# Optimization experiments

Hardware: AMD Instinct MI355X
Metric: run time of the kernel (lower is better)

## Reference

```python
import jax, jax.numpy as jnp
import numpy as np

D_MODEL = 1024; D_STATE = 64; D_CONV = 4; EXPAND = 2; HEADDIM = 128; NGROUPS = 1; CHUNK = 256
D_INNER = EXPAND * D_MODEL            # 2048
NHEADS = D_INNER // HEADDIM           # 16
CONV_DIM = D_INNER + 2 * NGROUPS * D_STATE   # 2176
D_IN_PROJ = 2 * D_INNER + 2 * NGROUPS * D_STATE + NHEADS  # 4240
B = 4; G = 256; L = 2048
EPS = 1e-5


def setup_inputs() -> dict:
    key = jax.random.key(0)
    ks = jax.random.split(key, 12)
    def nrm(k, shape, s=0.02):
        return jax.random.normal(k, shape, jnp.float32) * s
    return dict(
        local_repr=jax.random.normal(ks[0], (B, L, D_MODEL), jnp.float32),
        global_repr=jax.random.normal(ks[1], (B, G, D_MODEL), jnp.float32),
        norm1_w=jnp.ones((D_MODEL,), jnp.float32), norm1_b=jnp.zeros((D_MODEL,), jnp.float32),
        norm2_w=jnp.ones((D_MODEL,), jnp.float32), norm2_b=jnp.zeros((D_MODEL,), jnp.float32),
        norm3_w=jnp.ones((D_MODEL,), jnp.float32), norm3_b=jnp.zeros((D_MODEL,), jnp.float32),
        in_proj_w=nrm(ks[2], (D_IN_PROJ, D_MODEL)),
        conv_w=nrm(ks[3], (CONV_DIM, D_CONV), 0.2),
        conv_b=jnp.zeros((CONV_DIM,), jnp.float32),
        dt_bias=jnp.log(jnp.expm1(jax.random.uniform(ks[4], (NHEADS,), jnp.float32, 1e-3, 0.1))),
        A_log=jnp.log(jax.random.uniform(ks[5], (NHEADS,), jnp.float32, 1.0, 16.0)),
        D_skip=jnp.ones((NHEADS,), jnp.float32),
        ssd_norm_w=jnp.ones((D_INNER,), jnp.float32),
        out_proj_w=nrm(ks[6], (D_MODEL, D_INNER)),
        ffn_w1=nrm(ks[7], (D_MODEL // 2, D_MODEL)),
        ffn_b1=jnp.zeros((D_MODEL // 2,), jnp.float32),
        ffn_w2=nrm(ks[8], (D_MODEL, D_MODEL // 2)),
        ffn_b2=jnp.zeros((D_MODEL,), jnp.float32),
    )


def _ln(x, w, b):
    mu = jnp.mean(x, axis=-1, keepdims=True)
    var = jnp.mean((x - mu) ** 2, axis=-1, keepdims=True)
    return (x - mu) * jax.lax.rsqrt(var + EPS) * w + b


def _segsum(a):
    # a: (..., T) -> (..., T, T) lower-triangular sums a[j+1..i]
    T = a.shape[-1]
    cs = jnp.cumsum(a, axis=-1)
    diff = cs[..., :, None] - cs[..., None, :]
    mask = jnp.tril(jnp.ones((T, T), bool))
    return jnp.where(mask, diff, -jnp.inf)


def _ssd(xdt, a_dt, Bh, Ch):
    # xdt: (b,t,h,p) = x*dt ; a_dt: (b,t,h) = dt*A ; Bh,Ch: (b,t,h,n)
    b, t, h, p = xdt.shape
    n = Bh.shape[-1]
    c = t // CHUNK
    X = xdt.reshape(b, c, CHUNK, h, p)
    Bc = Bh.reshape(b, c, CHUNK, h, n)
    Cc = Ch.reshape(b, c, CHUNK, h, n)
    Ac = a_dt.reshape(b, c, CHUNK, h).transpose(0, 3, 1, 2)  # (b,h,c,k)
    A_cum = jnp.cumsum(Ac, axis=-1)
    Lm = jnp.exp(_segsum(Ac))                                # (b,h,c,k,k)
    Y_diag = jnp.einsum('bckhn,bcshn,bhcks,bcshp->bckhp', Cc, Bc, Lm, X)
    decay_states = jnp.exp(A_cum[..., -1:] - A_cum)          # (b,h,c,k)
    states = jnp.einsum('bckhn,bhck,bckhp->bchpn', Bc, decay_states, X)
    A_last = jnp.pad(A_cum[..., -1], ((0, 0), (0, 0), (1, 0)))
    decay_chunk = jnp.exp(_segsum(A_last))                   # (b,h,c+1,c+1)
    states = jnp.concatenate([jnp.zeros_like(states[:, :1]), states], axis=1)
    new_states = jnp.einsum('bhzc,bchpn->bzhpn', decay_chunk, states)
    states_in = new_states[:, :-1]                           # (b,c,h,p,n)
    out_decay = jnp.exp(A_cum)                               # (b,h,c,k)
    Y_off = jnp.einsum('bckhn,bchpn,bhck->bckhp', Cc, states_in, out_decay)
    return (Y_diag + Y_off).reshape(b, t, h, p)


def _mamba2(x, in_proj_w, conv_w, conv_b, dt_bias, A_log, D_skip, ssd_norm_w, out_proj_w):
    b, t, _ = x.shape
    zxbcdt = x @ in_proj_w.T                                  # (b,t,D_IN_PROJ)
    z = zxbcdt[..., :D_INNER]
    xBC = zxbcdt[..., D_INNER:D_INNER + CONV_DIM]
    dt = jax.nn.softplus(zxbcdt[..., D_INNER + CONV_DIM:] + dt_bias)  # (b,t,h)
    # causal depthwise conv1d, kernel D_CONV
    xp = jnp.pad(xBC, ((0, 0), (D_CONV - 1, 0), (0, 0)))
    xBC = sum(xp[:, i:i + t, :] * conv_w[:, i] for i in range(D_CONV)) + conv_b
    xBC = jax.nn.silu(xBC)
    xs = xBC[..., :D_INNER].reshape(b, t, NHEADS, HEADDIM)
    Bm = xBC[..., D_INNER:D_INNER + NGROUPS * D_STATE].reshape(b, t, NGROUPS, D_STATE)
    Cm = xBC[..., D_INNER + NGROUPS * D_STATE:].reshape(b, t, NGROUPS, D_STATE)
    rep = NHEADS // NGROUPS
    Bh = jnp.repeat(Bm, rep, axis=2)
    Ch = jnp.repeat(Cm, rep, axis=2)
    A = -jnp.exp(A_log)                                       # (h,)
    Y = _ssd(xs * dt[..., None], dt * A, Bh, Ch)
    y = Y + D_skip[None, None, :, None] * xs
    y = y.reshape(b, t, D_INNER)
    # gated RMSNorm (norm_before_gate=False)
    y = y * jax.nn.silu(z)
    y = y * jax.lax.rsqrt(jnp.mean(y * y, axis=-1, keepdims=True) + EPS) * ssd_norm_w
    return y @ out_proj_w.T


def reference(local_repr, global_repr, norm1_w, norm1_b, norm2_w, norm2_b, norm3_w, norm3_b,
              in_proj_w, conv_w, conv_b, dt_bias, A_log, D_skip, ssd_norm_w, out_proj_w,
              ffn_w1, ffn_b1, ffn_w2, ffn_b2):
    local_n = _ln(local_repr, norm1_w, norm1_b)
    global_n = _ln(global_repr, norm2_w, norm2_b)
    x = jnp.concatenate([global_n, local_n], axis=1)          # (B, G+L, D)
    x = _mamba2(x, in_proj_w, conv_w, conv_b, dt_bias, A_log, D_skip, ssd_norm_w, out_proj_w)
    x = x[:, -local_n.shape[1]:, :] + local_n
    x = _ln(x, norm3_w, norm3_b)
    h = jax.nn.gelu(x @ ffn_w1.T + ffn_b1, approximate=False)
    return (h @ ffn_w2.T + ffn_b2) + x
```

## Files before the change

### kernel.cpp

```cpp
#include <hip/hip_runtime.h>
#include <math.h>

#define B_ 4
#define L_ 2048
#define G_ 256
#define T_ 2304
#define DM 1024
#define DINNER 2048
#define NH 16
#define HD 128
#define NSTATE 64
#define CONVD 2176
#define DPROJ 4240
#define NPROJ_PAD 4352
#define NCHUNK 9
#define CK 256
#define EPSV 1e-5f
#define CROWS 16
#define CONVBLKS 612

typedef unsigned short bf16t;
using bf16x8 = __attribute__((ext_vector_type(8))) short;
using f32x4  = __attribute__((ext_vector_type(4))) float;

__device__ __forceinline__ float bf2f(bf16t u) {
  return __uint_as_float(((unsigned int)u) << 16);
}
__device__ __forceinline__ bf16t f2bf(float f) {
  unsigned int u = __float_as_uint(f);
  u += 0x7FFFu + ((u >> 16) & 1u);
  return (bf16t)(u >> 16);
}

__device__ __forceinline__ void g2lds16(const bf16t* g, short* l) {
  __builtin_amdgcn_global_load_lds(
      (const __attribute__((address_space(1))) unsigned int*)g,
      (__attribute__((address_space(3))) unsigned int*)l, 16, 0, 0);
}

__device__ __forceinline__ int2 xcd_swz(int tiles_n) {
  int gx = gridDim.x, gy = gridDim.y;
  int id = blockIdx.y * gx + blockIdx.x;
  int cpx = (gx * gy) >> 3;
  int L = (id & 7) * cpx + (id >> 3);
  return make_int2(L % tiles_n, L / tiles_n);
}

__device__ __forceinline__ float2 block_reduce2(float a, float b) {
  __shared__ float sa[4], sb[4];
  #pragma unroll
  for (int off = 32; off > 0; off >>= 1) {
    a += __shfl_down(a, off, 64);
    b += __shfl_down(b, off, 64);
  }
  int lane = threadIdx.x & 63, wid = threadIdx.x >> 6;
  if (lane == 0) { sa[wid] = a; sb[wid] = b; }
  __syncthreads();
  return make_float2(sa[0] + sa[1] + sa[2] + sa[3], sb[0] + sb[1] + sb[2] + sb[3]);
}

__global__ __launch_bounds__(256) void ln_cvt_kernel(
    const float* __restrict__ localr, const float* __restrict__ globalr,
    const float* __restrict__ w1, const float* __restrict__ b1,
    const float* __restrict__ w2, const float* __restrict__ b2,
    bf16t* __restrict__ x, const float* __restrict__ inpw,
    bf16t* __restrict__ inpw_bf) {
  int blk = blockIdx.x;
  if (blk < B_ * T_) {
    int t = blk % T_, b = blk / T_;
    const float *src, *w, *bb;
    if (t < G_) { src = globalr + ((long)b * G_ + t) * DM;        w = w2; bb = b2; }
    else        { src = localr  + ((long)b * L_ + (t - G_)) * DM; w = w1; bb = b1; }
    int d = threadIdx.x * 4;
    float4 v = *(const float4*)&src[d];
    float s = v.x + v.y + v.z + v.w;
    float sq = v.x * v.x + v.y * v.y + v.z * v.z + v.w * v.w;
    float2 r2 = block_reduce2(s, sq);
    float mu = r2.x * (1.f / DM);
    float var = r2.y * (1.f / DM) - mu * mu;
    float rstd = rsqrtf(var + EPSV);
    float4 wv = *(const float4*)&w[d];
    float4 bv = *(const float4*)&bb[d];
    ushort4 o;
    o.x = f2bf((v.x - mu) * rstd * wv.x + bv.x);
    o.y = f2bf((v.y - mu) * rstd * wv.y + bv.y);
    o.z = f2bf((v.z - mu) * rstd * wv.z + bv.z);
    o.w = f2bf((v.w - mu) * rstd * wv.w + bv.w);
    *(ushort4*)&x[(long)blk * DM + d] = o;
  } else {
    long i = (long)(blk - B_ * T_) * 1024 + threadIdx.x * 4;
    const long nreal = (long)DPROJ * DM, ntot = (long)NPROJ_PAD * DM;
    if (i < ntot) {
      ushort4 o = {0, 0, 0, 0};
      if (i < nreal) {
        float4 v = *(const float4*)&inpw[i];
        o.x = f2bf(v.x); o.y = f2bf(v.y); o.z = f2bf(v.z); o.w = f2bf(v.w);
      }
      *(ushort4*)&inpw_bf[i] = o;
    }
  }
}

template<int EPI, bool OFFS, int K>
__global__ __launch_bounds__(512, 4) void gemm_wide(
    const bf16t* __restrict__ A, const bf16t* __restrict__ W,
    bf16t* __restrict__ Cb, bf16t* __restrict__ z, bf16t* __restrict__ xpre,
    float* __restrict__ dtr, const float* __restrict__ bias,
    const bf16t* __restrict__ res, float* __restrict__ Cf, int N) {
  __shared__ short LDS8[36864];
  int tid = threadIdx.x;
  int lane = tid & 63, w = tid >> 6;
  int wm = w >> 1, wn = w & 1;
  int l15 = lane & 15;
  int2 sz = xcd_swz(gridDim.x);
  int bn = sz.x * 128, bm = sz.y * 256;
  if (EPI == 0 && bn < DINNER && (bm % 2304) == 0) return;
  long bmA = OFFS ? ((long)(bm >> 11) * T_ + G_ + (bm & 2047)) : (long)bm;

  int csub = ((lane & 3) ^ ((lane >> 3) & 3)) * 8;
  const bf16t* srcA = A + (bmA + w * 16 + (lane >> 2)) * (long)K + csub;
  const bf16t* srcW = W + (long)(bn + w * 16 + (lane >> 2)) * K + csub;
  int stageDst = w * 512 + lane * 8;

  int off0 = l15 * 32 + (((lane >> 4) ^ ((l15 >> 1) & 3))) * 8;

  f32x4 acc[4][4] = {};
  bf16x8 af[4], bq[4];

#define STAGEA(gsrc, ldsoff) do { \
    g2lds16((gsrc), LDS8 + (ldsoff) + stageDst); \
    g2lds16((gsrc) + 128 * (long)K, LDS8 + (ldsoff) + stageDst + 4096); } while (0)
#define STAGEB(gsrc, ldsoff) g2lds16((gsrc), LDS8 + (ldsoff) + stageDst)

  STAGEA(srcA, 0);
  STAGEB(srcW, 24576);
  STAGEA(srcA + 32, 8192);
  STAGEB(srcW + 32, 24576 + 4096);
  asm volatile("s_waitcnt vmcnt(3)" ::: "memory");
  __builtin_amdgcn_s_barrier();

  const int nt = K >> 5;
  for (int t = 0; t < nt; ++t) {
    const short* aB = LDS8 + (t % 3) * 8192 + wm * 2048;
    const short* bB = LDS8 + 24576 + (t % 3) * 4096 + wn * 2048;
    int nsA = ((t + 2) % 3) * 8192;
    int nsB = 24576 + ((t + 2) % 3) * 4096;

    if (t + 2 < nt) {
      STAGEA(srcA + (t + 2) * 32, nsA);
      STAGEB(srcW + (t + 2) * 32, nsB);
    }
    #pragma unroll
    for (int mi = 0; mi < 4; mi++) af[mi] = *(const bf16x8*)&aB[mi * 512 + off0];
    #pragma unroll
    for (int ni = 0; ni < 4; ni++) bq[ni] = *(const bf16x8*)&bB[ni * 512 + off0];
    __builtin_amdgcn_s_setprio(1);
    #pragma unroll
    for (int mi = 0; mi < 4; mi++)
      #pragma unroll
      for (int ni = 0; ni < 4; ni++)
        acc[mi][ni] = __builtin_amdgcn_mfma_f32_16x16x32_bf16(af[mi], bq[ni], acc[mi][ni], 0, 0, 0);
    __builtin_amdgcn_s_setprio(0);
    if (t + 2 < nt)      asm volatile("s_waitcnt vmcnt(3)" ::: "memory");
    else if (t + 1 < nt) asm volatile("s_waitcnt vmcnt(0)" ::: "memory");
    __builtin_amdgcn_s_barrier();
  }
#undef STAGEA
#undef STAGEB

  if (EPI == 0 && bn == 4224) {
    if (wn == 0) {
      #pragma unroll
      for (int mi = 0; mi < 4; mi++)
        #pragma unroll
        for (int r = 0; r < 4; r++) {
          int row = bm + wm * 64 + mi * 16 + (lane >> 4) * 4 + r;
          dtr[(long)row * NH + l15] = acc[mi][0][r];
        }
    }
    return;
  }

  if (EPI == 2) {
    float* Cs32 = (float*)LDS8;
    #pragma unroll
    for (int pass = 0; pass < 4; pass++) {
      __syncthreads();
      if (wm == pass) {
        #pragma unroll
        for (int mi = 0; mi < 4; mi++)
          #pragma unroll
          for (int ni = 0; ni < 4; ni++)
            #pragma unroll
            for (int r = 0; r < 4; r++)
              Cs32[(mi * 16 + (lane >> 4) * 4 + r) * 136 + wn * 64 + ni * 16 + l15] =
                  acc[mi][ni][r];
      }
      __syncthreads();
      #pragma unroll
      for (int q = 0; q < 2; q++) {
        int idx = q * 512 + tid;
        int row = idx >> 4, cg = (idx & 15) * 8;
        long grow = bm + pass * 64 + row; int gcol = bn + cg;
        float4 v0 = *(float4*)&Cs32[row * 136 + cg];
        float4 v1 = *(float4*)&Cs32[row * 136 + cg + 4];
        float4 b0 = *(const float4*)&bias[gcol];
        float4 b1 = *(const float4*)&bias[gcol + 4];
        bf16x8 rv = *(const bf16x8*)&res[grow * (long)N + gcol];
        v0.x += b0.x + bf2f((bf16t)rv[0]); v0.y += b0.y + bf2f((bf16t)rv[1]);
        v0.z += b0.z + bf2f((bf16t)rv[2]); v0.w += b0.w + bf2f((bf16t)rv[3]);
        v1.x += b1.x + bf2f((bf16t)rv[4]); v1.y += b1.y + bf2f((bf16t)rv[5]);
        v1.z += b1.z + bf2f((bf16t)rv[6]); v1.w += b1.w + bf2f((bf16t)rv[7]);
        *(float4*)&Cf[grow * (long)N + gcol] = v0;
        *(float4*)&Cf[grow * (long)N + gcol + 4] = v1;
      }
    }
    return;
  }

  bf16t* Cs = (bf16t*)LDS8;
  #pragma unroll
  for (int pass = 0; pass < 2; pass++) {
    __syncthreads();
    if ((wm >> 1) == pass) {
      #pragma unroll
      for (int mi = 0; mi < 4; mi++)
        #pragma unroll
        for (int ni = 0; ni < 4; ni++)
          #pragma unroll
          for (int r = 0; r < 4; r++)
            Cs[((wm & 1) * 64 + mi * 16 + (lane >> 4) * 4 + r) * 136 + wn * 64 + ni * 16 + l15] =
                f2bf(acc[mi][ni][r]);
    }
    __syncthreads();
    #pragma unroll
    for (int q = 0; q < 4; q++) {
      int idx = q * 512 + tid;
      int row = idx >> 4, cg = idx & 15;
      int gcol = bn + cg * 8;
      long grow = bm + pass * 128 + row;
      bf16x8 v = *(bf16x8*)&Cs[row * 136 + cg * 8];
      if (EPI == 0) {
        if (gcol < DINNER) *(bf16x8*)&z[grow * DINNER + gcol] = v;
        else               *(bf16x8*)&xpre[grow * CONVD + (gcol - DINNER)] = v;
      } else {
        *(bf16x8*)&Cb[grow * (long)N + gcol] = v;
      }
    }
  }
}

template<int EPI>
__global__ __launch_bounds__(256) void gemm_mfma(
    const bf16t* __restrict__ A, const bf16t* __restrict__ W,
    const float* __restrict__ bias, const bf16t* __restrict__ res,
    float* __restrict__ Cf, bf16t* __restrict__ Cb,
    int N, int K) {
  __shared__ __align__(16) short LDS[128 * 136];
  short* As = LDS;
  short* Ws = LDS + 128 * 32;
  int tid = threadIdx.x;
  int lane = tid & 63, w = tid >> 6;
  int wr = w >> 1, wc = w & 1;
  int2 sz = xcd_swz(gridDim.x);
  int bn = sz.x * 128, bm = sz.y * 128;

  int r1 = tid >> 2,         s1 = (((tid & 3) ^ ((r1 >> 1) & 3))) * 8;
  int r2 = (tid + 256) >> 2, s2 = (((tid & 3) ^ ((r2 >> 1) & 3))) * 8;
  const bf16t* gA1 = A + (long)(bm + r1) * K + s1;
  const bf16t* gA2 = A + (long)(bm + r2) * K + s2;
  const bf16t* gW1 = W + (long)(bn + r1) * K + s1;
  const bf16t* gW2 = W + (long)(bn + r2) * K + s2;
  short* lA1 = As + tid * 8;
  short* lA2 = As + (tid + 256) * 8;
  short* lW1 = Ws + tid * 8;
  short* lW2 = Ws + (tid + 256) * 8;

  int arow = wr * 64 + (lane & 15);
  int brow = wc * 64 + (lane & 15);
  int koff = (((lane >> 4) ^ (((lane & 15) >> 1) & 3))) * 8;

  f32x4 acc[4][4] = {};
  for (int k0 = 0; k0 < K; k0 += 32) {
    g2lds16(gA1 + k0, lA1);
    g2lds16(gA2 + k0, lA2);
    g2lds16(gW1 + k0, lW1);
    g2lds16(gW2 + k0, lW2);
    __syncthreads();
    bf16x8 af[4], bf[4];
    #pragma unroll
    for (int mi = 0; mi < 4; mi++) af[mi] = *(bf16x8*)&As[(arow + mi * 16) * 32 + koff];
    #pragma unroll
    for (int ni = 0; ni < 4; ni++) bf[ni] = *(bf16x8*)&Ws[(brow + ni * 16) * 32 + koff];
    #pragma unroll
    for (int mi = 0; mi < 4; mi++)
      #pragma unroll
      for (int ni = 0; ni < 4; ni++)
        acc[mi][ni] = __builtin_amdgcn_mfma_f32_16x16x32_bf16(af[mi], bf[ni], acc[mi][ni], 0, 0, 0);
    __syncthreads();
  }

  int rb = wr * 64 + (lane >> 4) * 4;
  int cb = wc * 64 + (lane & 15);

  __syncthreads();
  bf16t* Cs = (bf16t*)LDS;
  #pragma unroll
  for (int mi = 0; mi < 4; mi++)
    #pragma unroll
    for (int ni = 0; ni < 4; ni++)
      #pragma unroll
      for (int r = 0; r < 4; r++) {
        float v = acc[mi][ni][r];
        if (EPI == 2) {
          v += bias[bn + cb + ni * 16];
          v = 0.5f * v * (1.f + erff(v * 0.70710678118f));
        }
        Cs[(rb + mi * 16 + r) * 136 + cb + ni * 16] = f2bf(v);
      }
  __syncthreads();
  #pragma unroll
  for (int pass = 0; pass < 8; pass++) {
    int row = pass * 16 + (tid >> 4);
    int col = (tid & 15) * 8;
    bf16x8 vv = *(bf16x8*)&Cs[row * 136 + col];
    long grow = bm + row; int gcol = bn + col;
    *(bf16x8*)&Cb[grow * N + gcol] = vv;
  }
}

__global__ __launch_bounds__(256) void conv_cumsum_kernel(
    const bf16t* __restrict__ xpre, const float* __restrict__ cw,
    const float* __restrict__ cb, bf16t* __restrict__ out,
    const float* __restrict__ dtraw, const float* __restrict__ dt_bias,
    const float* __restrict__ A_log, float* __restrict__ dt,
    float* __restrict__ Acum) {
  if (blockIdx.x < CONVBLKS) {
    int gt = blockIdx.x * 256 + threadIdx.x;
    int cg = gt % 272; int rt = gt / 272;
    int c0 = cg * 8;
    long r0 = (long)rt * CROWS;
    int t0 = (int)(r0 % T_);

    float wreg[4][8];
    #pragma unroll
    for (int j = 0; j < 8; j++) {
      float4 wa = *(const float4*)&cw[(c0 + j) * 4];
      wreg[0][j] = wa.x; wreg[1][j] = wa.y; wreg[2][j] = wa.z; wreg[3][j] = wa.w;
    }
    float4 cb0 = *(const float4*)&cb[c0];
    float4 cb1 = *(const float4*)&cb[c0 + 4];
    float bias[8] = {cb0.x, cb0.y, cb0.z, cb0.w, cb1.x, cb1.y, cb1.z, cb1.w};

    bf16x8 win[4];
    #pragma unroll
    for (int i = 0; i < 3; i++) {
      if (t0 - 3 + i >= 0) win[i] = *(const bf16x8*)&xpre[(r0 - 3 + i) * CONVD + c0];
      else                 win[i] = bf16x8{0,0,0,0,0,0,0,0};
    }

    #pragma unroll
    for (int k = 0; k < CROWS; k++) {
      win[3] = *(const bf16x8*)&xpre[(r0 + k) * CONVD + c0];
      float acc[8];
      #pragma unroll
      for (int j = 0; j < 8; j++) acc[j] = bias[j];
      #pragma unroll
      for (int i = 0; i < 4; i++)
        #pragma unroll
        for (int j = 0; j < 8; j++)
          acc[j] += bf2f((bf16t)win[i][j]) * wreg[i][j];
      bf16x8 o;
      #pragma unroll
      for (int j = 0; j < 8; j++) {
        float s = acc[j] / (1.f + __expf(-acc[j]));
        o[j] = (short)f2bf(s);
      }
      *(bf16x8*)&out[(r0 + k) * CONVD + c0] = o;
      win[0] = win[1]; win[1] = win[2]; win[2] = win[3];
    }
  } else {
    int bid = blockIdx.x - CONVBLKS;
    int c = bid % NCHUNK; int hh = bid / NCHUNK;
    int h = hh % NH; int b = hh / NH;
    int k = threadIdx.x;
    float a = -__expf(A_log[h]);
    long t = (long)b * T_ + c * CK + k;
    float v0 = dtraw[t * NH + h] + dt_bias[h];
    float dtv = (v0 > 20.f) ? v0 : log1pf(__expf(v0));
    dt[t * NH + h] = dtv;
    float v = dtv * a;
    __shared__ float buf[2][CK];
    int cur = 0;
    buf[0][k] = v; __syncthreads();
    for (int off = 1; off < CK; off <<= 1) {
      float tv = buf[cur][k];
      if (k >= off) tv += buf[cur][k - off];
      buf[1 - cur][k] = tv; cur ^= 1; __syncthreads();
    }
    Acum[(long)bid * CK + k] = buf[cur][k];
  }
}

__global__ __launch_bounds__(256) void chunk_states_kernel(
    const bf16t* __restrict__ xbc, const float* __restrict__ dt,
    const float* __restrict__ Acum, float* __restrict__ cs) {
  int bid = blockIdx.x;
  int h = bid & 15; int bc = bid >> 4;
  int c = bc & 7; int b = bc >> 3;
  int tid = threadIdx.x;
  int lane = tid & 63, w = tid >> 6;
  long tch = (long)b * T_ + c * CK;
  int acb = ((b * NH + h) * NCHUNK + c) * CK;
  float Alast = Acum[acb + CK - 1];

  __shared__ bf16t Xt[128][72];
  __shared__ bf16t Bt[64][72];
  __shared__ float wkv[256];
  wkv[tid] = __expf(Alast - Acum[acb + tid]) * dt[(tch + tid) * NH + h];

  f32x4 acc[8] = {};
  for (int kb = 0; kb < 4; kb++) {
    int s0 = kb * 64;
    __syncthreads();
    for (int e = tid; e < 16 * 32; e += 256) {
      int s4 = (e & 15) * 4, p4 = e >> 4;
      const bf16t* base = &xbc[(tch + s0 + s4) * CONVD + h * HD + p4 * 4];
      ushort4 u0 = *(const ushort4*)(base);
      ushort4 u1 = *(const ushort4*)(base + CONVD);
      ushort4 u2 = *(const ushort4*)(base + 2 * CONVD);
      ushort4 u3 = *(const ushort4*)(base + 3 * CONVD);
      float w0 = wkv[s0 + s4], w1 = wkv[s0 + s4 + 1];
      float w2 = wkv[s0 + s4 + 2], w3 = wkv[s0 + s4 + 3];
      ushort4 pk;
      pk.x = f2bf(bf2f(u0.x) * w0); pk.y = f2bf(bf2f(u1.x) * w1);
      pk.z = f2bf(bf2f(u2.x) * w2); pk.w = f2bf(bf2f(u3.x) * w3);
      *(ushort4*)&Xt[p4 * 4 + 0][s4] = pk;
      pk.x = f2bf(bf2f(u0.y) * w0); pk.y = f2bf(bf2f(u1.y) * w1);
      pk.z = f2bf(bf2f(u2.y) * w2); pk.w = f2bf(bf2f(u3.y) * w3);
      *(ushort4*)&Xt[p4 * 4 + 1][s4] = pk;
      pk.x = f2bf(bf2f(u0.z) * w0); pk.y = f2bf(bf2f(u1.z) * w1);
      pk.z = f2bf(bf2f(u2.z) * w2); pk.w = f2bf(bf2f(u3.z) * w3);
      *(ushort4*)&Xt[p4 * 4 + 2][s4] = pk;
      pk.x = f2bf(bf2f(u0.w) * w0); pk.y = f2bf(bf2f(u1.w) * w1);
      pk.z = f2bf(bf2f(u2.w) * w2); pk.w = f2bf(bf2f(u3.w) * w3);
      *(ushort4*)&Xt[p4 * 4 + 3][s4] = pk;
    }
    for (int e = tid; e < 16 * 16; e += 256) {
      int s4 = (e & 15) * 4, n4 = e >> 4;
      const bf16t* base = &xbc[(tch + s0 + s4) * CONVD + DINNER + n4 * 4];
      ushort4 u0 = *(const ushort4*)(base);
      ushort4 u1 = *(const ushort4*)(base + CONVD);
      ushort4 u2 = *(const ushort4*)(base + 2 * CONVD);
      ushort4 u3 = *(const ushort4*)(base + 3 * CONVD);
      ushort4 pk;
      pk.x = u0.x; pk.y = u1.x; pk.z = u2.x; pk.w = u3.x;
      *(ushort4*)&Bt[n4 * 4 + 0][s4] = pk;
      pk.x = u0.y; pk.y = u1.y; pk.z = u2.y; pk.w = u3.y;
      *(ushort4*)&Bt[n4 * 4 + 1][s4] = pk;
      pk.x = u0.z; pk.y = u1.z; pk.z = u2.z; pk.w = u3.z;
      *(ushort4*)&Bt[n4 * 4 + 2][s4] = pk;
      pk.x = u0.w; pk.y = u1.w; pk.z = u2.w; pk.w = u3.w;
      *(ushort4*)&Bt[n4 * 4 + 3][s4] = pk;
    }
    __syncthreads();
    #pragma unroll
    for (int ks = 0; ks < 2; ks++) {
      int koff = (lane >> 4) * 8 + ks * 32;
      bf16x8 bfr = *(bf16x8*)&Bt[w * 16 + (lane & 15)][koff];
      #pragma unroll
      for (int mi = 0; mi < 8; mi++) {
        bf16x8 af = *(bf16x8*)&Xt[mi * 16 + (lane & 15)][koff];
        acc[mi] = __builtin_amdgcn_mfma_f32_16x16x32_bf16(af, bfr, acc[mi], 0, 0, 0);
      }
    }
  }
  int cbid = (b * NCHUNK + c) * NH + h;
  float* out = cs + (long)cbid * HD * NSTATE;
  int n = w * 16 + (lane & 15);
  #pragma unroll
  for (int mi = 0; mi < 8; mi++) {
    #pragma unroll
    for (int r = 0; r < 4; r++) {
      int p = mi * 16 + (lane >> 4) * 4 + r;
      out[p * NSTATE + n] = acc[mi][r];
    }
  }
}

__global__ __launch_bounds__(256) void state_pass_kernel(
    float* __restrict__ cs, const float* __restrict__ Acum) {
  int bh = blockIdx.x;
  int b = bh / NH, h = bh % NH;
  int e0 = blockIdx.y * 1024 + threadIdx.x;
  for (int q = 0; q < 4; q++) {
    int e = e0 + q * 256;
    float s = 0.f;
    for (int c = 0; c < NCHUNK; c++) {
      long idx = ((long)(b * NCHUNK + c) * NH + h) * (HD * NSTATE) + e;
      if (c < NCHUNK - 1) {
        float tmp = cs[idx];
        cs[idx] = s;
        float g = __expf(Acum[((b * NH + h) * NCHUNK + c) * CK + CK - 1]);
        s = s * g + tmp;
      } else {
        cs[idx] = s;
      }
    }
  }
}

__global__ __launch_bounds__(256) void ssd_y_kernel(
    const bf16t* __restrict__ xbc, const float* __restrict__ dt,
    const float* __restrict__ Acum, const float* __restrict__ sin_,
    const float* __restrict__ Dskip, bf16t* __restrict__ Y) {
  int bid = blockIdx.x;
  int h = bid & 15; int bc = bid >> 4;
  int c = 1 + (bc & 7); int b = bc >> 3;
  int rt = blockIdx.y;
  int tid = threadIdx.x;
  int lane = tid & 63, w = tid >> 6;
  int wr = w >> 1, wc = w & 1;
  long tch = (long)b * T_ + c * CK;
  long tbase = tch + rt * 128;
  int acb = ((b * NH + h) * NCHUNK + c) * CK;

  __shared__ bf16t Cs[128][72];
  __shared__ bf16t Bs[64][72];
  __shared__ __align__(16) bf16t XtSm[2][128][72];
  bf16t (*Xt)[72] = XtSm[0];
  bf16t (*Sm)[72] = XtSm[1];
  __shared__ float Acv[256];
  __shared__ float dtv[256];

  for (int e = tid; e < 128 * 8; e += 256) {
    int row = e >> 3, seg = (e & 7) * 8;
    *(bf16x8*)&Cs[row][seg] =
        *(const bf16x8*)&xbc[(tbase + row) * CONVD + DINNER + NSTATE + seg];
  }
  Acv[tid] = Acum[acb + tid];
  dtv[tid] = dt[(tch + tid) * NH + h];
  const float* Ak = Acv + rt * 128;

  f32x4 acc[4][4] = {};
  int nsb = 2 * (rt + 1);
  for (int sb = 0; sb < nsb; sb++) {
    int s0 = sb * 64;
    __syncthreads();
    for (int e = tid; e < 64 * 8; e += 256) {
      int row = e >> 3, seg = (e & 7) * 8;
      *(bf16x8*)&Bs[row][seg] =
          *(const bf16x8*)&xbc[(tch + s0 + row) * CONVD + DINNER + seg];
    }
    for (int e = tid; e < 16 * 32; e += 256) {
      int s4 = (e & 15) * 4, p4 = e >> 4;
      const bf16t* base = &xbc[(tch + s0 + s4) * CONVD + h * HD + p4 * 4];
      ushort4 u0 = *(const ushort4*)(base);
      ushort4 u1 = *(const ushort4*)(base + CONVD);
      ushort4 u2 = *(const ushort4*)(base + 2 * CONVD);
      ushort4 u3 = *(const ushort4*)(base + 3 * CONVD);
      float d0 = dtv[s0 + s4], d1 = dtv[s0 + s4 + 1];
      float d2 = dtv[s0 + s4 + 2], d3 = dtv[s0 + s4 + 3];
      ushort4 pk;
      pk.x = f2bf(bf2f(u0.x) * d0); pk.y = f2bf(bf2f(u1.x) * d1);
      pk.z = f2bf(bf2f(u2.x) * d2); pk.w = f2bf(bf2f(u3.x) * d3);
      *(ushort4*)&Xt[p4 * 4 + 0][s4] = pk;
      pk.x = f2bf(bf2f(u0.y) * d0); pk.y = f2bf(bf2f(u1.y) * d1);
      pk.z = f2bf(bf2f(u2.y) * d2); pk.w = f2bf(bf2f(u3.y) * d3);
      *(ushort4*)&Xt[p4 * 4 + 1][s4] = pk;
      pk.x = f2bf(bf2f(u0.z) * d0); pk.y = f2bf(bf2f(u1.z) * d1);
      pk.z = f2bf(bf2f(u2.z) * d2); pk.w = f2bf(bf2f(u3.z) * d3);
      *(ushort4*)&Xt[p4 * 4 + 2][s4] = pk;
      pk.x = f2bf(bf2f(u0.w) * d0); pk.y = f2bf(bf2f(u1.w) * d1);
      pk.z = f2bf(bf2f(u2.w) * d2); pk.w = f2bf(bf2f(u3.w) * d3);
      *(ushort4*)&Xt[p4 * 4 + 3][s4] = pk;
    }
    __syncthreads();
    {
      f32x4 sacc[2][4] = {};
      int rw0 = w * 32;
      #pragma unroll
      for (int ks = 0; ks < 2; ks++) {
        int koff = (lane >> 4) * 8 + ks * 32;
        bf16x8 a0 = *(bf16x8*)&Cs[rw0 + (lane & 15)][koff];
        bf16x8 a1 = *(bf16x8*)&Cs[rw0 + 16 + (lane & 15)][koff];
        #pragma unroll
        for (int ni = 0; ni < 4; ni++) {
          bf16x8 bfr = *(bf16x8*)&Bs[ni * 16 + (lane & 15)][koff];
          sacc[0][ni] = __builtin_amdgcn_mfma_f32_16x16x32_bf16(a0, bfr, sacc[0][ni], 0, 0, 0);
          sacc[1][ni] = __builtin_amdgcn_mfma_f32_16x16x32_bf16(a1, bfr, sacc[1][ni], 0, 0, 0);
        }
      }
      #pragma unroll
      for (int mi = 0; mi < 2; mi++) {
        #pragma unroll
        for (int ni = 0; ni < 4; ni++) {
          #pragma unroll
          for (int r = 0; r < 4; r++) {
            int row = rw0 + mi * 16 + (lane >> 4) * 4 + r;
            int scol = ni * 16 + (lane & 15);
            int kglob = rt * 128 + row;
            int sglob = s0 + scol;
            float val = 0.f;
            if (sglob <= kglob) val = sacc[mi][ni][r] * __expf(Ak[row] - Acv[s0 + scol]);
            Sm[row][scol] = f2bf(val);
          }
        }
      }
    }
    __syncthreads();
    #pragma unroll
    for (int ks = 0; ks < 2; ks++) {
      int koff = (lane >> 4) * 8 + ks * 32;
      bf16x8 af[4], bfr[4];
      #pragma unroll
      for (int mi = 0; mi < 4; mi++) af[mi] = *(bf16x8*)&Sm[wr * 64 + mi * 16 + (lane & 15)][koff];
      #pragma unroll
      for (int ni = 0; ni < 4; ni++) bfr[ni] = *(bf16x8*)&Xt[wc * 64 + ni * 16 + (lane & 15)][koff];
      #pragma unroll
      for (int mi = 0; mi < 4; mi++)
        #pragma unroll
        for (int ni = 0; ni < 4; ni++)
          acc[mi][ni] = __builtin_amdgcn_mfma_f32_16x16x32_bf16(af[mi], bfr[ni], acc[mi][ni], 0, 0, 0);
    }
  }

  float ekr[16];
  #pragma unroll
  for (int mi = 0; mi < 4; mi++)
    #pragma unroll
    for (int r = 0; r < 4; r++)
      ekr[mi * 4 + r] = __expf(Ak[wr * 64 + mi * 16 + (lane >> 4) * 4 + r]);

  int cbid = (b * NCHUNK + c) * NH + h;
  const float* sinb = sin_ + (long)cbid * HD * NSTATE;
  #pragma unroll
  for (int ni = 0; ni < 4; ni++) {
    f32x4 offacc[4] = {};
    int p = wc * 64 + ni * 16 + (lane & 15);
    #pragma unroll
    for (int ks = 0; ks < 2; ks++) {
      int koff = (lane >> 4) * 8 + ks * 32;
      const float* srow = sinb + p * NSTATE + koff;
      float4 sa = *(const float4*)srow;
      float4 sbv = *(const float4*)(srow + 4);
      bf16x8 bfr;
      bfr[0] = (short)f2bf(sa.x);  bfr[1] = (short)f2bf(sa.y);
      bfr[2] = (short)f2bf(sa.z);  bfr[3] = (short)f2bf(sa.w);
      bfr[4] = (short)f2bf(sbv.x); bfr[5] = (short)f2bf(sbv.y);
      bfr[6] = (short)f2bf(sbv.z); bfr[7] = (short)f2bf(sbv.w);
      #pragma unroll
      for (int mi = 0; mi < 4; mi++) {
        bf16x8 af = *(bf16x8*)&Cs[wr * 64 + mi * 16 + (lane & 15)][koff];
        offacc[mi] = __builtin_amdgcn_mfma_f32_16x16x32_bf16(af, bfr, offacc[mi], 0, 0, 0);
      }
    }
    #pragma unroll
    for (int mi = 0; mi < 4; mi++)
      #pragma unroll
      for (int r = 0; r < 4; r++)
        acc[mi][ni][r] += ekr[mi * 4 + r] * offacc[mi][r];
  }

  float dsk = Dskip[h];
  float* Sf = (float*)&XtSm[0][0][0];
  #pragma unroll
  for (int rh = 0; rh < 2; rh++) {
    __syncthreads();
    if (wr == rh) {
      #pragma unroll
      for (int mi = 0; mi < 4; mi++)
        #pragma unroll
        for (int ni = 0; ni < 4; ni++)
          #pragma unroll
          for (int r = 0; r < 4; r++)
            Sf[(mi * 16 + (lane >> 4) * 4 + r) * 130 + wc * 64 + ni * 16 + (lane & 15)] =
                acc[mi][ni][r];
    }
    __syncthreads();
    #pragma unroll
    for (int g = 0; g < 4; g++) {
      int idx = g * 256 + tid;
      int row = idx >> 4, cg = (idx & 15) * 8;
      long t = tbase + rh * 64 + row;
      bf16x8 xv = *(const bf16x8*)&xbc[t * CONVD + h * HD + cg];
      bf16x8 o;
      #pragma unroll
      for (int j = 0; j < 8; j++)
        o[j] = (short)f2bf(Sf[row * 130 + cg + j] + dsk * bf2f((bf16t)xv[j]));
      *(bf16x8*)&Y[t * DINNER + h * HD + cg] = o;
    }
  }
}

__global__ __launch_bounds__(256) void gate_rms_cvt_kernel(
    const bf16t* __restrict__ z, const float* __restrict__ nw,
    bf16t* __restrict__ Y,
    const float* __restrict__ outw, const float* __restrict__ f1w,
    const float* __restrict__ f2w, bf16t* __restrict__ o_out,
    bf16t* __restrict__ o_f1, bf16t* __restrict__ o_f2) {
  int blk = blockIdx.x;
  if (blk < B_ * L_) {
    long r = (long)(blk >> 11) * T_ + G_ + (blk & 2047);
    const bf16t* zrow = z + r * DINNER;
    bf16t* yrow = Y + r * DINNER;
    int tid = threadIdx.x;
    int d = tid * 8;
    bf16x8 zu = *(const bf16x8*)&zrow[d];
    bf16x8 yu = *(const bf16x8*)&yrow[d];
    float v[8]; float sq = 0.f;
    #pragma unroll
    for (int j = 0; j < 8; j++) {
      float z0 = bf2f((bf16t)zu[j]);
      float y0 = bf2f((bf16t)yu[j]) * (z0 / (1.f + __expf(-z0)));
      v[j] = y0; sq += y0 * y0;
    }
    float2 r2 = block_reduce2(sq, 0.f);
    float rms = rsqrtf(r2.x * (1.f / DINNER) + EPSV);
    float4 nw0 = *(const float4*)&nw[d];
    float4 nw1 = *(const float4*)&nw[d + 4];
    float nn[8] = {nw0.x, nw0.y, nw0.z, nw0.w, nw1.x, nw1.y, nw1.z, nw1.w};
    bf16x8 o;
    #pragma unroll
    for (int j = 0; j < 8; j++) o[j] = (short)f2bf(v[j] * rms * nn[j]);
    *(bf16x8*)&yrow[d] = o;
  } else {
    long i = (long)(blk - B_ * L_) * 1024 + threadIdx.x * 4;
    const long n1 = (long)DM * DINNER;
    const long n2 = (long)(DM / 2) * DM;
    const float* src; bf16t* dst; long off;
    if (i < n1) { src = outw; dst = o_out; off = i; }
    else if (i < n1 + n2) { src = f1w; dst = o_f1; off = i - n1; }
    else { src = f2w; dst = o_f2; off = i - n1 - n2; }
    float4 v = *(const float4*)&src[off];
    ushort4 o;
    o.x = f2bf(v.x); o.y = f2bf(v.y); o.z = f2bf(v.z); o.w = f2bf(v.w);
    *(ushort4*)&dst[off] = o;
  }
}

__global__ __launch_bounds__(256) void res_ln3_kernel(
    const bf16t* __restrict__ mfull, const bf16t* __restrict__ x,
    const float* __restrict__ w3, const float* __restrict__ b3,
    bf16t* __restrict__ x2) {
  int rl = blockIdx.x;
  int tl = rl & 2047, b = rl >> 11;
  long rt = (long)b * T_ + G_ + tl;
  const bf16t* m = mfull + (long)rl * DM;
  const bf16t* xr = x + rt * DM;
  int tid = threadIdx.x;
  int d = tid * 4;
  ushort4 mu4 = *(const ushort4*)&m[d];
  ushort4 xu4 = *(const ushort4*)&xr[d];
  float v[4];
  v[0] = bf2f(mu4.x) + bf2f(xu4.x);
  v[1] = bf2f(mu4.y) + bf2f(xu4.y);
  v[2] = bf2f(mu4.z) + bf2f(xu4.z);
  v[3] = bf2f(mu4.w) + bf2f(xu4.w);
  float s = v[0] + v[1] + v[2] + v[3];
  float sq = v[0]*v[0] + v[1]*v[1] + v[2]*v[2] + v[3]*v[3];
  float2 r2 = block_reduce2(s, sq);
  float mu = r2.x * (1.f / DM);
  float var = r2.y * (1.f / DM) - mu * mu;
  float rstd = rsqrtf(var + EPSV);
  float4 w4 = *(const float4*)&w3[d];
  float4 b4 = *(const float4*)&b3[d];
  ushort4 o;
  o.x = f2bf((v[0] - mu) * rstd * w4.x + b4.x);
  o.y = f2bf((v[1] - mu) * rstd * w4.y + b4.y);
  o.z = f2bf((v[2] - mu) * rstd * w4.z + b4.z);
  o.w = f2bf((v[3] - mu) * rstd * w4.w + b4.w);
  *(ushort4*)&x2[(long)rl * DM + d] = o;
}

extern "C" void kernel_launch(void* const* d_in, const int* in_sizes, int n_in,
                              void* d_out, int out_size, void* d_ws, size_t ws_size,
                              hipStream_t stream) {
  const float* localr = (const float*)d_in[0];
  const float* globalr= (const float*)d_in[1];
  const float* n1w = (const float*)d_in[2];
  const float* n1b = (const float*)d_in[3];
  const float* n2w = (const float*)d_in[4];
  const float* n2b = (const float*)d_in[5];
  const float* n3w = (const float*)d_in[6];
  const float* n3b = (const float*)d_in[7];
  const float* inpw= (const float*)d_in[8];
  const float* convw=(const float*)d_in[9];
  const float* convb=(const float*)d_in[10];
  const float* dtb = (const float*)d_in[11];
  const float* alog= (const float*)d_in[12];
  const float* dskp= (const float*)d_in[13];
  const float* ssdw= (const float*)d_in[14];
  const float* outw= (const float*)d_in[15];
  const float* f1w = (const float*)d_in[16];
  const float* f1b = (const float*)d_in[17];
  const float* f2w = (const float*)d_in[18];
  const float* f2b = (const float*)d_in[19];

  char* ws = (char*)d_ws;
  bf16t* x     = (bf16t*)(ws + 0);
  bf16t* z     = (bf16t*)(ws + 18874368);
  bf16t* mfull = (bf16t*)(ws + 18874368);
  bf16t* xpre  = (bf16t*)(ws + 56623104);
  bf16t* Yb    = (bf16t*)(ws + 56623104);
  float* dtraw = (float*)(ws + 96731136);
  float* dt    = (float*)(ws + 97320960);
  float* Acum  = (float*)(ws + 97910784);
  bf16t* xbc   = (bf16t*)(ws + 98500608);
  bf16t* x2bf  = (bf16t*)(ws + 98500608);
  bf16t* hbuf  = (bf16t*)(ws + 115277824);
  bf16t* outw_bf = (bf16t*)(ws + 123666432);
  bf16t* f1w_bf  = (bf16t*)(ws + 127860736);
  bf16t* f2w_bf  = (bf16t*)(ws + 128909312);
  float* cs    = (float*)(ws + 138608640);
  bf16t* inpw_bf = (bf16t*)(ws + 138608640);

  ln_cvt_kernel<<<B_ * T_ + 4352, 256, 0, stream>>>(
      localr, globalr, n1w, n1b, n2w, n2b, x, inpw, inpw_bf);

  gemm_wide<0, false, 1024><<<dim3(NPROJ_PAD / 128, (B_ * T_) / 256), 512, 0, stream>>>(
      x, inpw_bf, nullptr, z, xpre, dtraw, nullptr, nullptr, nullptr, NPROJ_PAD);

  conv_cumsum_kernel<<<CONVBLKS + B_ * NH * NCHUNK, 256, 0, stream>>>(
      xpre, convw, convb, xbc, dtraw, dtb, alog, dt, Acum);

  chunk_states_kernel<<<B_ * (NCHUNK - 1) * NH, 256, 0, stream>>>(xbc, dt, Acum, cs);

  state_pass_kernel<<<dim3(B_ * NH, 8), 256, 0, stream>>>(cs, Acum);

  ssd_y_kernel<<<dim3(B_ * (NCHUNK - 1) * NH, 2), 256, 0, stream>>>(
      xbc, dt, Acum, cs, dskp, Yb);

  gate_rms_cvt_kernel<<<B_ * L_ + 3072, 256, 0, stream>>>(
      z, ssdw, Yb, outw, f1w, f2w, outw_bf, f1w_bf, f2w_bf);

  gemm_wide<1, true, 2048><<<dim3(DM / 128, (B_ * L_) / 256), 512, 0, stream>>>(
      Yb, outw_bf, mfull, nullptr, nullptr, nullptr, nullptr, nullptr, nullptr, DM);

  res_ln3_kernel<<<B_ * L_, 256, 0, stream>>>(mfull, x, n3w, n3b, x2bf);

  gemm_mfma<2><<<dim3((DM / 2) / 128, (B_ * L_) / 128), 256, 0, stream>>>(
      x2bf, f1w_bf, f1b, nullptr, nullptr, hbuf, DM / 2, DM);

  gemm_wide<2, false, 512><<<dim3(DM / 128, (B_ * L_) / 256), 512, 0, stream>>>(
      hbuf, f2w_bf, nullptr, nullptr, nullptr, nullptr, f2b, x2bf, (float*)d_out, DM);
}
```

Measured before the change: 447.6 us.

## Add 128x128-tile triple-buffered GEMM for out_proj and FFN2, flatten ssd_y grid

Adds a new gemm_wide128 kernel that uses 256 threads and 128x128 output tiles, a three-stage LDS ring and direct global-to-LDS loads, with launch bounds allowing three blocks per CU. The out_proj and second FFN GEMMs switch to it, so their grids double in block count for better CU fill on the N=1024 outputs. The ssd_y launch is flattened to 1D so the two row tiles of a chunk sit in adjacent blocks. In exchange, each block reuses less data per tile and loads more operand bytes per FLOP.

New measurement: 551.9 us. 1.23x slower.

```diff
diff --git a/kernel.cpp b/kernel.cpp
--- a/kernel.cpp
+++ b/kernel.cpp
@@ -181,10 +181,105 @@
     return;
   }
 
+  bf16t* Cs = (bf16t*)LDS8;
+  #pragma unroll
+  for (int pass = 0; pass < 2; pass++) {
+    __syncthreads();
+    if ((wm >> 1) == pass) {
+      #pragma unroll
+      for (int mi = 0; mi < 4; mi++)
+        #pragma unroll
+        for (int ni = 0; ni < 4; ni++)
+          #pragma unroll
+          for (int r = 0; r < 4; r++)
+            Cs[((wm & 1) * 64 + mi * 16 + (lane >> 4) * 4 + r) * 136 + wn * 64 + ni * 16 + l15] =
+                f2bf(acc[mi][ni][r]);
+    }
+    __syncthreads();
+    #pragma unroll
+    for (int q = 0; q < 4; q++) {
+      int idx = q * 512 + tid;
+      int row = idx >> 4, cg = idx & 15;
+      int gcol = bn + cg * 8;
+      long grow = bm + pass * 128 + row;
+      bf16x8 v = *(bf16x8*)&Cs[row * 136 + cg * 8];
+      if (EPI == 0) {
+        if (gcol < DINNER) *(bf16x8*)&z[grow * DINNER + gcol] = v;
+        else               *(bf16x8*)&xpre[grow * CONVD + (gcol - DINNER)] = v;
+      } else {
+        *(bf16x8*)&Cb[grow * (long)N + gcol] = v;
+      }
+    }
+  }
+}
+
+template<int EPI, bool OFFS, int K>
+__global__ __launch_bounds__(256, 3) void gemm_wide128(
+    const bf16t* __restrict__ A, const bf16t* __restrict__ W,
+    bf16t* __restrict__ Cb, const float* __restrict__ bias,
+    const bf16t* __restrict__ res, float* __restrict__ Cf, int N) {
+  __shared__ short LDS8[24576];
+  int tid = threadIdx.x;
+  int lane = tid & 63, w = tid >> 6;
+  int wm = w >> 1, wn = w & 1;
+  int l15 = lane & 15;
+  int2 sz = xcd_swz(gridDim.x);
+  int bn = sz.x * 128, bm = sz.y * 128;
+  long bmA = OFFS ? ((long)(bm >> 11) * T_ + G_ + (bm & 2047)) : (long)bm;
+
+  int csub = ((lane & 3) ^ ((lane >> 3) & 3)) * 8;
+  const bf16t* srcA = A + (bmA + w * 16 + (lane >> 2)) * (long)K + csub;
+  const bf16t* srcW = W + (long)(bn + w * 16 + (lane >> 2)) * K + csub;
+  int stageDst = w * 512 + lane * 8;
+
+  int off0 = l15 * 32 + (((lane >> 4) ^ ((l15 >> 1) & 3))) * 8;
+
+  f32x4 acc[4][4] = {};
+  bf16x8 af[4], bq[4];
+
+#define STG(gsrc, ldsoff) do { \
+    g2lds16((gsrc), LDS8 + (ldsoff) + stageDst); \
+    g2lds16((gsrc) + 64 * (long)K, LDS8 + (ldsoff) + stageDst + 2048); } while (0)
+
+  STG(srcA, 0);
+  STG(srcW, 12288);
+  STG(srcA + 32, 4096);
+  STG(srcW + 32, 12288 + 4096);
+  asm volatile("s_waitcnt vmcnt(4)" ::: "memory");
+  __builtin_amdgcn_s_barrier();
+
+  const int nt = K >> 5;
+  for (int t = 0; t < nt; ++t) {
+    const short* aB = LDS8 + (t % 3) * 4096 + wm * 2048;
+    const short* bB = LDS8 + 12288 + (t % 3) * 4096 + wn * 2048;
+    int nsA = ((t + 2) % 3) * 4096;
+    int nsB = 12288 + ((t + 2) % 3) * 4096;
+
+    if (t + 2 < nt) {
+      STG(srcA + (t + 2) * 32, nsA);
+      STG(srcW + (t + 2) * 32, nsB);
+    }
+    #pragma unroll
+    for (int mi = 0; mi < 4; mi++) af[mi] = *(const bf16x8*)&aB[mi * 512 + off0];
+    #pragma unroll
+    for (int ni = 0; ni < 4; ni++) bq[ni] = *(const bf16x8*)&bB[ni * 512 + off0];
+    __builtin_amdgcn_s_setprio(1);
+    #pragma unroll
+    for (int mi = 0; mi < 4; mi++)
+      #pragma unroll
+      for (int ni = 0; ni < 4; ni++)
+        acc[mi][ni] = __builtin_amdgcn_mfma_f32_16x16x32_bf16(af[mi], bq[ni], acc[mi][ni], 0, 0, 0);
+    __builtin_amdgcn_s_setprio(0);
+    if (t + 2 < nt)      asm volatile("s_waitcnt vmcnt(4)" ::: "memory");
+    else if (t + 1 < nt) asm volatile("s_waitcnt vmcnt(0)" ::: "memory");
+    __builtin_amdgcn_s_barrier();
+  }
+#undef STG
+
   if (EPI == 2) {
     float* Cs32 = (float*)LDS8;
     #pragma unroll
-    for (int pass = 0; pass < 4; pass++) {
+    for (int pass = 0; pass < 2; pass++) {
       __syncthreads();
       if (wm == pass) {
         #pragma unroll
@@ -198,8 +293,8 @@
       }
       __syncthreads();
       #pragma unroll
-      for (int q = 0; q < 2; q++) {
-        int idx = q * 512 + tid;
+      for (int q = 0; q < 4; q++) {
+        int idx = q * 256 + tid;
         int row = idx >> 4, cg = (idx & 15) * 8;
         long grow = bm + pass * 64 + row; int gcol = bn + cg;
         float4 v0 = *(float4*)&Cs32[row * 136 + cg];
@@ -219,34 +314,21 @@
   }
 
   bf16t* Cs = (bf16t*)LDS8;
+  __syncthreads();
   #pragma unroll
-  for (int pass = 0; pass < 2; pass++) {
-    __syncthreads();
-    if ((wm >> 1) == pass) {
-      #pragma unroll
-      for (int mi = 0; mi < 4; mi++)
-        #pragma unroll
-        for (int ni = 0; ni < 4; ni++)
-          #pragma unroll
-          for (int r = 0; r < 4; r++)
-            Cs[((wm & 1) * 64 + mi * 16 + (lane >> 4) * 4 + r) * 136 + wn * 64 + ni * 16 + l15] =
-                f2bf(acc[mi][ni][r]);
-    }
-    __syncthreads();
-    #pragma unroll
-    for (int q = 0; q < 4; q++) {
-      int idx = q * 512 + tid;
-      int row = idx >> 4, cg = idx & 15;
-      int gcol = bn + cg * 8;
-      long grow = bm + pass * 128 + row;
-      bf16x8 v = *(bf16x8*)&Cs[row * 136 + cg * 8];
-      if (EPI == 0) {
-        if (gcol < DINNER) *(bf16x8*)&z[grow * DINNER + gcol] = v;
-        else               *(bf16x8*)&xpre[grow * CONVD + (gcol - DINNER)] = v;
-      } else {
-        *(bf16x8*)&Cb[grow * (long)N + gcol] = v;
-      }
-    }
+  for (int mi = 0; mi < 4; mi++)
+    #pragma unroll
+    for (int ni = 0; ni < 4; ni++)
+      #pragma unroll
+      for (int r = 0; r < 4; r++)
+        Cs[(wm * 64 + mi * 16 + (lane >> 4) * 4 + r) * 136 + wn * 64 + ni * 16 + l15] =
+            f2bf(acc[mi][ni][r]);
+  __syncthreads();
+  #pragma unroll
+  for (int p = 0; p < 8; p++) {
+    int idx = p * 256 + tid;
+    int row = idx >> 4, cg = idx & 15;
+    *(bf16x8*)&Cb[(long)(bm + row) * N + bn + cg * 8] = *(bf16x8*)&Cs[row * 136 + cg * 8];
   }
 }
 
@@ -514,10 +596,11 @@
     const bf16t* __restrict__ xbc, const float* __restrict__ dt,
     const float* __restrict__ Acum, const float* __restrict__ sin_,
     const float* __restrict__ Dskip, bf16t* __restrict__ Y) {
-  int bid = blockIdx.x;
+  int bid2 = blockIdx.x;
+  int rt = bid2 & 1;
+  int bid = bid2 >> 1;
   int h = bid & 15; int bc = bid >> 4;
   int c = 1 + (bc & 7); int b = bc >> 3;
-  int rt = blockIdx.y;
   int tid = threadIdx.x;
   int lane = tid & 63, w = tid >> 6;
   int wr = w >> 1, wc = w & 1;
@@ -828,20 +911,20 @@
 
   state_pass_kernel<<<dim3(B_ * NH, 8), 256, 0, stream>>>(cs, Acum);
 
-  ssd_y_kernel<<<dim3(B_ * (NCHUNK - 1) * NH, 2), 256, 0, stream>>>(
+  ssd_y_kernel<<<B_ * (NCHUNK - 1) * NH * 2, 256, 0, stream>>>(
       xbc, dt, Acum, cs, dskp, Yb);
 
   gate_rms_cvt_kernel<<<B_ * L_ + 3072, 256, 0, stream>>>(
       z, ssdw, Yb, outw, f1w, f2w, outw_bf, f1w_bf, f2w_bf);
 
-  gemm_wide<1, true, 2048><<<dim3(DM / 128, (B_ * L_) / 256), 512, 0, stream>>>(
-      Yb, outw_bf, mfull, nullptr, nullptr, nullptr, nullptr, nullptr, nullptr, DM);
+  gemm_wide128<1, true, 2048><<<dim3(DM / 128, (B_ * L_) / 128), 256, 0, stream>>>(
+      Yb, outw_bf, mfull, nullptr, nullptr, nullptr, DM);
 
   res_ln3_kernel<<<B_ * L_, 256, 0, stream>>>(mfull, x, n3w, n3b, x2bf);
 
   gemm_mfma<2><<<dim3((DM / 2) / 128, (B_ * L_) / 128), 256, 0, stream>>>(
       x2bf, f1w_bf, f1b, nullptr, nullptr, hbuf, DM / 2, DM);
 
-  gemm_wide<2, false, 512><<<dim3(DM / 128, (B_ * L_) / 256), 512, 0, stream>>>(
-      hbuf, f2w_bf, nullptr, nullptr, nullptr, nullptr, f2b, x2bf, (float*)d_out, DM);
-}
+  gemm_wide128<2, false, 512><<<dim3(DM / 128, (B_ * L_) / 128), 256, 0, stream>>>(
+      hbuf, f2w_bf, nullptr, f2b, x2bf, (float*)d_out, DM);
+}
```
